# Optimization experiments

Hardware: AMD Instinct MI355X
Metric: run time of the kernel (lower is better)

The kernel has to match this reference:

```python
import jax, jax.numpy as jnp
import numpy as np

N_NODES = 100000
N_EDGES = 1000000
N_GRAPHS = 128
IN_DIM, HID, LAT, N_LAYERS = 32, 64, 32, 3


def setup_inputs() -> dict:
    key = jax.random.key(0)
    ks = jax.random.split(key, 10)
    x = jax.random.normal(ks[0], (N_NODES, IN_DIM), dtype=jnp.float32)
    edge_index = jax.random.randint(ks[1], (2, N_EDGES), 0, N_NODES, dtype=jnp.int64)
    batch = jnp.sort(jax.random.randint(ks[2], (N_NODES,), 0, N_GRAPHS, dtype=jnp.int64))
    s_in = 1.0 / np.sqrt(IN_DIM)
    s_h = 1.0 / np.sqrt(HID)
    return {
        "x": x,
        "edge_index": edge_index,
        "batch": batch,
        "w_in": jax.random.normal(ks[3], (IN_DIM, HID), dtype=jnp.float32) * s_in,
        "b_in": jnp.zeros((HID,), jnp.float32),
        "w1": jax.random.normal(ks[4], (N_LAYERS, HID, HID), dtype=jnp.float32) * s_h,
        "b1": jnp.zeros((N_LAYERS, HID), jnp.float32),
        "w2": jax.random.normal(ks[5], (N_LAYERS, HID, HID), dtype=jnp.float32) * s_h,
        "b2": jnp.zeros((N_LAYERS, HID), jnp.float32),
        "w_fc": jax.random.normal(ks[6], (HID, LAT), dtype=jnp.float32) * s_h,
        "b_fc": jnp.zeros((LAT,), jnp.float32),
    }


def reference(x, edge_index, batch, w_in, b_in, w1, b1, w2, b2, w_fc, b_fc):
    # Input projection: [N, in] -> [N, H]
    h = x @ w_in + b_in
    src, dst = edge_index[0], edge_index[1]
    for i in range(N_LAYERS):
        h_skip = h
        # GINConv (eps=0): aggregate neighbor sum then MLP
        agg = jax.ops.segment_sum(h[src], dst, num_segments=N_NODES)  # [N, H]
        m = h + agg
        m = jax.nn.relu(m @ w1[i] + b1[i])
        m = jax.nn.relu(m @ w2[i] + b2[i])
        # dropout is identity in eval mode; residual skip
        h = m + h_skip
    # global_add_pool over graphs
    pooled = jax.ops.segment_sum(h, batch, num_segments=N_GRAPHS)  # [G, H]
    return pooled @ w_fc + b_fc
```

## Files before the change

### kernel.cpp

```cpp
#include <hip/hip_runtime.h>

#define N_NODES 100000
#define N_EDGES 1000000
#define N_GRAPHS 128
#define IN_DIM 32
#define HID 64
#define LAT 32
#define N_LAYERS 3

#define MPAD 68
#define NB_SUM ((N_NODES + 255) / 256)

__global__ __launch_bounds__(256) void proj_kernel(
    const float* __restrict__ x, const float* __restrict__ w_in,
    const float* __restrict__ b_in, float* __restrict__ h) {
    __shared__ float ws[IN_DIM * HID];
    __shared__ float xs[4 * IN_DIM];
    int tid = threadIdx.x;
    for (int i = tid; i < IN_DIM * HID / 4; i += 256)
        ((float4*)ws)[i] = ((const float4*)w_in)[i];
    if (tid < 32) {
        int r = tid >> 3, c4 = tid & 7;
        int nn = blockIdx.x * 4 + r;
        float4 v = make_float4(0.f, 0.f, 0.f, 0.f);
        if (nn < N_NODES) v = ((const float4*)(x + (size_t)nn * IN_DIM))[c4];
        ((float4*)xs)[tid] = v;
    }
    __syncthreads();
    int w = tid >> 6, j = tid & 63;
    int n = blockIdx.x * 4 + w;
    if (n >= N_NODES) return;
    float acc = b_in[j];
#pragma unroll
    for (int k = 0; k < IN_DIM; k += 4) {
        float4 xv = *(const float4*)&xs[w * IN_DIM + k];
        acc += xv.x * ws[(k + 0) * HID + j];
        acc += xv.y * ws[(k + 1) * HID + j];
        acc += xv.z * ws[(k + 2) * HID + j];
        acc += xv.w * ws[(k + 3) * HID + j];
    }
    h[(size_t)n * HID + j] = acc;
}

__global__ __launch_bounds__(256) void hist_kernel(const int* __restrict__ ei,
                                                   int* __restrict__ counts) {
    int e = blockIdx.x * 256 + threadIdx.x;
    if (e < N_EDGES) atomicAdd(&counts[ei[N_EDGES + e]], 1);
}

__global__ __launch_bounds__(256) void block_sum_kernel(
    const int* __restrict__ counts, int* __restrict__ bsums) {
    __shared__ int sd[4];
    int i = blockIdx.x * 256 + threadIdx.x;
    int v = (i < N_NODES) ? counts[i] : 0;
#pragma unroll
    for (int off = 32; off >= 1; off >>= 1) v += __shfl_down(v, off);
    int lane = threadIdx.x & 63, w = threadIdx.x >> 6;
    if (lane == 0) sd[w] = v;
    __syncthreads();
    if (threadIdx.x == 0) bsums[blockIdx.x] = sd[0] + sd[1] + sd[2] + sd[3];
}

__global__ __launch_bounds__(256) void scan_bsums_kernel(
    const int* __restrict__ bsums, int* __restrict__ bofs, int nb) {
    __shared__ int tmp[256];
    __shared__ int carry;
    int tid = threadIdx.x;
    if (tid == 0) carry = 0;
    __syncthreads();
    for (int base = 0; base < nb; base += 256) {
        int v = (base + tid < nb) ? bsums[base + tid] : 0;
        tmp[tid] = v;
        __syncthreads();
        for (int off = 1; off < 256; off <<= 1) {
            int t = (tid >= off) ? tmp[tid - off] : 0;
            __syncthreads();
            tmp[tid] += t;
            __syncthreads();
        }
        if (base + tid < nb) bofs[base + tid] = carry + tmp[tid] - v;
        __syncthreads();
        if (tid == 255) carry += tmp[255];
        __syncthreads();
    }
}

__global__ __launch_bounds__(256) void offsets_kernel(
    const int* __restrict__ counts, const int* __restrict__ bofs,
    int* __restrict__ offsets, int* __restrict__ cursor) {
    __shared__ int tmp[256];
    int tid = threadIdx.x;
    int i = blockIdx.x * 256 + tid;
    int v = (i < N_NODES) ? counts[i] : 0;
    tmp[tid] = v;
    __syncthreads();
    for (int off = 1; off < 256; off <<= 1) {
        int t = (tid >= off) ? tmp[tid - off] : 0;
        __syncthreads();
        tmp[tid] += t;
        __syncthreads();
    }
    int excl = tmp[tid] - v + bofs[blockIdx.x];
    if (i < N_NODES) {
        offsets[i] = excl;
        cursor[i] = excl;
        if (i == N_NODES - 1) offsets[N_NODES] = excl + v;
    }
}

__global__ __launch_bounds__(256) void fill_kernel(const int* __restrict__ ei,
                                                   int* __restrict__ cursor,
                                                   int* __restrict__ srcs) {
    int e = blockIdx.x * 256 + threadIdx.x;
    if (e < N_EDGES) {
        int d = ei[N_EDGES + e];
        int p = atomicAdd(&cursor[d], 1);
        srcs[p] = ei[e];
    }
}

__global__ __launch_bounds__(256) void gather_kernel(
    const int* __restrict__ offsets, const int* __restrict__ srcs,
    const float* __restrict__ h, float* __restrict__ agg) {
    int w = threadIdx.x >> 6, j = threadIdx.x & 63;
    int n = blockIdx.x * 4 + w;
    if (n >= N_NODES) return;
    int beg = offsets[n], end = offsets[n + 1];
    float acc0 = 0.f, acc1 = 0.f, acc2 = 0.f, acc3 = 0.f;
    for (int c = beg; c < end; c += 64) {
        int myS = (c + j < end) ? srcs[c + j] : 0;
        int m = min(64, end - c);
        int i = 0;
        for (; i + 3 < m; i += 4) {
            int s0 = __shfl(myS, i);
            int s1 = __shfl(myS, i + 1);
            int s2 = __shfl(myS, i + 2);
            int s3 = __shfl(myS, i + 3);
            acc0 += h[(size_t)s0 * HID + j];
            acc1 += h[(size_t)s1 * HID + j];
            acc2 += h[(size_t)s2 * HID + j];
            acc3 += h[(size_t)s3 * HID + j];
        }
        for (; i < m; i++) acc0 += h[(size_t)__shfl(myS, i) * HID + j];
    }
    agg[(size_t)n * HID + j] = acc0 + acc1 + acc2 + acc3;
}

__global__ __launch_bounds__(512) void mlp_kernel(
    float* __restrict__ h, const float* __restrict__ agg,
    const float* __restrict__ w1, const float* __restrict__ b1,
    const float* __restrict__ w2, const float* __restrict__ b2) {
    __shared__ float w1s[HID * HID];
    __shared__ float w2s[HID * HID];
    __shared__ float ms[64 * MPAD];
    int tid = threadIdx.x;
    int row0 = blockIdx.x * 64;
    for (int i = tid; i < HID * HID / 4; i += 512) {
        ((float4*)w1s)[i] = ((const float4*)w1)[i];
        ((float4*)w2s)[i] = ((const float4*)w2)[i];
    }
#pragma unroll
    for (int i = 0; i < 2; i++) {
        int f = tid + i * 512;
        int r = f >> 4, c4 = f & 15;
        int n = row0 + r;
        float4 mv = make_float4(0.f, 0.f, 0.f, 0.f);
        if (n < N_NODES) {
            float4 h4 = ((const float4*)(h + (size_t)n * HID))[c4];
            float4 a4 = ((const float4*)(agg + (size_t)n * HID))[c4];
            mv = make_float4(h4.x + a4.x, h4.y + a4.y, h4.z + a4.z, h4.w + a4.w);
        }
        *(float4*)&ms[r * MPAD + c4 * 4] = mv;
    }
    __syncthreads();

    int ty = tid >> 4, tx = tid & 15;
    int r0 = ty * 2, c0 = tx * 4;

    float4 a0, a1;
#define GEMM_LDS(WS)                                                          \
    do {                                                                      \
        a0 = make_float4(0.f, 0.f, 0.f, 0.f); a1 = a0;                        \
        _Pragma("unroll 4")                                                   \
        for (int k0 = 0; k0 < HID; k0 += 4) {                                 \
            float4 m0 = *(const float4*)&ms[(r0 + 0) * MPAD + k0];            \
            float4 m1 = *(const float4*)&ms[(r0 + 1) * MPAD + k0];            \
            float4 w0 = *(const float4*)&WS[(k0 + 0) * HID + c0];             \
            float4 w1v = *(const float4*)&WS[(k0 + 1) * HID + c0];            \
            float4 w2v = *(const float4*)&WS[(k0 + 2) * HID + c0];            \
            float4 w3v = *(const float4*)&WS[(k0 + 3) * HID + c0];            \
            a0.x += m0.x * w0.x + m0.y * w1v.x + m0.z * w2v.x + m0.w * w3v.x; \
            a0.y += m0.x * w0.y + m0.y * w1v.y + m0.z * w2v.y + m0.w * w3v.y; \
            a0.z += m0.x * w0.z + m0.y * w1v.z + m0.z * w2v.z + m0.w * w3v.z; \
            a0.w += m0.x * w0.w + m0.y * w1v.w + m0.z * w2v.w + m0.w * w3v.w; \
            a1.x += m1.x * w0.x + m1.y * w1v.x + m1.z * w2v.x + m1.w * w3v.x; \
            a1.y += m1.x * w0.y + m1.y * w1v.y + m1.z * w2v.y + m1.w * w3v.y; \
            a1.z += m1.x * w0.z + m1.y * w1v.z + m1.z * w2v.z + m1.w * w3v.z; \
            a1.w += m1.x * w0.w + m1.y * w1v.w + m1.z * w2v.w + m1.w * w3v.w; \
        }                                                                     \
    } while (0)

    GEMM_LDS(w1s);

    float4 bv1 = *(const float4*)&b1[c0];
    float4 t0 = make_float4(fmaxf(a0.x + bv1.x, 0.f), fmaxf(a0.y + bv1.y, 0.f),
                            fmaxf(a0.z + bv1.z, 0.f), fmaxf(a0.w + bv1.w, 0.f));
    float4 t1 = make_float4(fmaxf(a1.x + bv1.x, 0.f), fmaxf(a1.y + bv1.y, 0.f),
                            fmaxf(a1.z + bv1.z, 0.f), fmaxf(a1.w + bv1.w, 0.f));

    __syncthreads();
    *(float4*)&ms[(r0 + 0) * MPAD + c0] = t0;
    *(float4*)&ms[(r0 + 1) * MPAD + c0] = t1;
    __syncthreads();

    GEMM_LDS(w2s);

    float4 bv2 = *(const float4*)&b2[c0];
#pragma unroll
    for (int i = 0; i < 2; i++) {
        int n = row0 + r0 + i;
        if (n < N_NODES) {
            float4 av = (i == 0) ? a0 : a1;
            float4 hold = *(const float4*)(h + (size_t)n * HID + c0);
            float4 o;
            o.x = fmaxf(av.x + bv2.x, 0.f) + hold.x;
            o.y = fmaxf(av.y + bv2.y, 0.f) + hold.y;
            o.z = fmaxf(av.z + bv2.z, 0.f) + hold.z;
            o.w = fmaxf(av.w + bv2.w, 0.f) + hold.w;
            *(float4*)(h + (size_t)n * HID + c0) = o;
        }
    }
#undef GEMM_LDS
}

__global__ __launch_bounds__(256) void pool_kernel(
    const float* __restrict__ h, const int* __restrict__ batch,
    float* __restrict__ pooled) {
    int tid = threadIdx.x;
    int w = tid >> 6, j = tid & 63;
    int n0 = blockIdx.x * 256 + w * 64;
    if (n0 >= N_NODES) return;
    int nend = min(n0 + 64, N_NODES);
    float acc = 0.f;
    int cur = batch[n0];
    for (int n = n0; n < nend; n++) {
        int b = batch[n];
        if (b != cur) {
            atomicAdd(&pooled[cur * HID + j], acc);
            acc = 0.f;
            cur = b;
        }
        acc += h[(size_t)n * HID + j];
    }
    atomicAdd(&pooled[cur * HID + j], acc);
}

__global__ __launch_bounds__(256) void final_kernel(
    const float* __restrict__ pooled, const float* __restrict__ w_fc,
    const float* __restrict__ b_fc, float* __restrict__ out) {
    int gid = blockIdx.x * 256 + threadIdx.x;
    if (gid >= N_GRAPHS * LAT) return;
    int g = gid >> 5, j = gid & 31;
    float acc = b_fc[j];
#pragma unroll
    for (int k = 0; k < HID; k++)
        acc += pooled[g * HID + k] * w_fc[k * LAT + j];
    out[gid] = acc;
}

extern "C" void kernel_launch(void* const* d_in, const int* in_sizes, int n_in,
                              void* d_out, int out_size, void* d_ws,
                              size_t ws_size, hipStream_t stream) {
    const float* x     = (const float*)d_in[0];
    const int*   ei    = (const int*)d_in[1];
    const int*   batch = (const int*)d_in[2];
    const float* w_in  = (const float*)d_in[3];
    const float* b_in  = (const float*)d_in[4];
    const float* w1    = (const float*)d_in[5];
    const float* b1    = (const float*)d_in[6];
    const float* w2    = (const float*)d_in[7];
    const float* b2    = (const float*)d_in[8];
    const float* w_fc  = (const float*)d_in[9];
    const float* b_fc  = (const float*)d_in[10];
    float* out = (float*)d_out;

    float* h       = (float*)d_ws;
    float* agg     = h + (size_t)N_NODES * HID;
    float* pooled  = agg + (size_t)N_NODES * HID;
    int*   offsets = (int*)(pooled + N_GRAPHS * HID);
    int*   srcs    = offsets + (N_NODES + 2);
    int* counts = (int*)agg;
    int* cursor = counts + N_NODES;
    int* bsums  = cursor + N_NODES;
    int* bofs   = bsums + (NB_SUM + 1);

    proj_kernel<<<(N_NODES + 3) / 4, 256, 0, stream>>>(x, w_in, b_in, h);

    hipMemsetAsync(counts, 0, N_NODES * sizeof(int), stream);
    hist_kernel<<<(N_EDGES + 255) / 256, 256, 0, stream>>>(ei, counts);
    block_sum_kernel<<<NB_SUM, 256, 0, stream>>>(counts, bsums);
    scan_bsums_kernel<<<1, 256, 0, stream>>>(bsums, bofs, NB_SUM);
    offsets_kernel<<<NB_SUM, 256, 0, stream>>>(counts, bofs, offsets, cursor);
    fill_kernel<<<(N_EDGES + 255) / 256, 256, 0, stream>>>(ei, cursor, srcs);

    for (int i = 0; i < N_LAYERS; i++) {
        gather_kernel<<<(N_NODES + 3) / 4, 256, 0, stream>>>(offsets, srcs, h, agg);
        mlp_kernel<<<(N_NODES + 63) / 64, 512, 0, stream>>>(
            h, agg, w1 + (size_t)i * HID * HID, b1 + (size_t)i * HID,
            w2 + (size_t)i * HID * HID, b2 + (size_t)i * HID);
    }

    hipMemsetAsync(pooled, 0, N_GRAPHS * HID * sizeof(float), stream);
    pool_kernel<<<(N_NODES + 255) / 256, 256, 0, stream>>>(h, batch, pooled);
    final_kernel<<<(N_GRAPHS * LAT + 255) / 256, 256, 0, stream>>>(
        pooled, w_fc, b_fc, out);
}
```

Baseline: 480.9 us.

## Replace per-node CSR build with bucketed bin sort and LDS-atomic aggregation

Instead of building a full CSR (histogram, multi-kernel scan, atomic fill), edges are sorted into coarse buckets of 256 destination nodes using per-block LDS staging, packing the local destination and source into one int. Aggregation then runs one block per bucket, summing neighbor features into a shared-memory tile with LDS float atomics and writing the tile out coalesced. This aims to cut global atomic scatter and several launches from preprocessing. In exchange it uses 64 KB of LDS per block, launches few blocks, and adds LDS atomic contention and nondeterministic summation order.

```diff
diff --git a/kernel.cpp b/kernel.cpp
--- a/kernel.cpp
+++ b/kernel.cpp
@@ -9,7 +9,11 @@
 #define N_LAYERS 3
 
 #define MPAD 68
-#define NB_SUM ((N_NODES + 255) / 256)
+
+#define BSZ 256
+#define NBK ((N_NODES + BSZ - 1) / BSZ)
+#define EPB 16384
+#define NBIN_BLOCKS ((N_EDGES + EPB - 1) / EPB)
 
 __global__ __launch_bounds__(256) void proj_kernel(
     const float* __restrict__ x, const float* __restrict__ w_in,
@@ -42,108 +46,138 @@
     h[(size_t)n * HID + j] = acc;
 }
 
-__global__ __launch_bounds__(256) void hist_kernel(const int* __restrict__ ei,
-                                                   int* __restrict__ counts) {
-    int e = blockIdx.x * 256 + threadIdx.x;
-    if (e < N_EDGES) atomicAdd(&counts[ei[N_EDGES + e]], 1);
-}
-
-__global__ __launch_bounds__(256) void block_sum_kernel(
-    const int* __restrict__ counts, int* __restrict__ bsums) {
-    __shared__ int sd[4];
-    int i = blockIdx.x * 256 + threadIdx.x;
-    int v = (i < N_NODES) ? counts[i] : 0;
-#pragma unroll
-    for (int off = 32; off >= 1; off >>= 1) v += __shfl_down(v, off);
-    int lane = threadIdx.x & 63, w = threadIdx.x >> 6;
-    if (lane == 0) sd[w] = v;
-    __syncthreads();
-    if (threadIdx.x == 0) bsums[blockIdx.x] = sd[0] + sd[1] + sd[2] + sd[3];
-}
-
-__global__ __launch_bounds__(256) void scan_bsums_kernel(
-    const int* __restrict__ bsums, int* __restrict__ bofs, int nb) {
-    __shared__ int tmp[256];
-    __shared__ int carry;
-    int tid = threadIdx.x;
-    if (tid == 0) carry = 0;
-    __syncthreads();
-    for (int base = 0; base < nb; base += 256) {
-        int v = (base + tid < nb) ? bsums[base + tid] : 0;
-        tmp[tid] = v;
+__global__ __launch_bounds__(256) void bhist_kernel(const int* __restrict__ ei,
+                                                    int* __restrict__ bhist) {
+    __shared__ int hs[NBK];
+    for (int i = threadIdx.x; i < NBK; i += 256) hs[i] = 0;
+    __syncthreads();
+    int e = blockIdx.x * (256 * 16) + threadIdx.x;
+#pragma unroll
+    for (int k = 0; k < 16; k++, e += 256)
+        if (e < N_EDGES) atomicAdd(&hs[ei[N_EDGES + e] >> 8], 1);
+    __syncthreads();
+    for (int i = threadIdx.x; i < NBK; i += 256) {
+        int c = hs[i];
+        if (c) atomicAdd(&bhist[i], c);
+    }
+}
+
+__global__ __launch_bounds__(512) void bscan_kernel(const int* __restrict__ bhist,
+                                                    int* __restrict__ bstart,
+                                                    int* __restrict__ bcursor) {
+    __shared__ int sc[512];
+    int tid = threadIdx.x;
+    int v = (tid < NBK) ? bhist[tid] : 0;
+    sc[tid] = v;
+    __syncthreads();
+    for (int off = 1; off < 512; off <<= 1) {
+        int t = (tid >= off) ? sc[tid - off] : 0;
         __syncthreads();
-        for (int off = 1; off < 256; off <<= 1) {
-            int t = (tid >= off) ? tmp[tid - off] : 0;
-            __syncthreads();
-            tmp[tid] += t;
-            __syncthreads();
-        }
-        if (base + tid < nb) bofs[base + tid] = carry + tmp[tid] - v;
+        sc[tid] += t;
         __syncthreads();
-        if (tid == 255) carry += tmp[255];
+    }
+    if (tid < NBK) {
+        int ex = sc[tid] - v;
+        bstart[tid] = ex;
+        bcursor[tid] = ex;
+    }
+    if (tid == 0) bstart[NBK] = N_EDGES;
+}
+
+__global__ __launch_bounds__(512) void binsort_kernel(const int* __restrict__ ei,
+                                                      int* __restrict__ bcursor,
+                                                      int* __restrict__ tmp) {
+    __shared__ int hist[NBK];
+    __shared__ int lofs[NBK + 1];
+    __shared__ int cur[NBK];
+    __shared__ int gbase[NBK];
+    __shared__ int sc[512];
+    __shared__ int stage[EPB];
+    int tid = threadIdx.x;
+    int e0 = blockIdx.x * EPB;
+    int nE = min(EPB, N_EDGES - e0);
+    for (int i = tid; i < NBK; i += 512) hist[i] = 0;
+    __syncthreads();
+    for (int i = tid; i < nE; i += 512)
+        atomicAdd(&hist[ei[N_EDGES + e0 + i] >> 8], 1);
+    __syncthreads();
+    int v = (tid < NBK) ? hist[tid] : 0;
+    sc[tid] = v;
+    __syncthreads();
+    for (int off = 1; off < 512; off <<= 1) {
+        int t = (tid >= off) ? sc[tid - off] : 0;
         __syncthreads();
-    }
-}
-
-__global__ __launch_bounds__(256) void offsets_kernel(
-    const int* __restrict__ counts, const int* __restrict__ bofs,
-    int* __restrict__ offsets, int* __restrict__ cursor) {
-    __shared__ int tmp[256];
-    int tid = threadIdx.x;
-    int i = blockIdx.x * 256 + tid;
-    int v = (i < N_NODES) ? counts[i] : 0;
-    tmp[tid] = v;
-    __syncthreads();
-    for (int off = 1; off < 256; off <<= 1) {
-        int t = (tid >= off) ? tmp[tid - off] : 0;
+        sc[tid] += t;
         __syncthreads();
-        tmp[tid] += t;
-        __syncthreads();
-    }
-    int excl = tmp[tid] - v + bofs[blockIdx.x];
-    if (i < N_NODES) {
-        offsets[i] = excl;
-        cursor[i] = excl;
-        if (i == N_NODES - 1) offsets[N_NODES] = excl + v;
-    }
-}
-
-__global__ __launch_bounds__(256) void fill_kernel(const int* __restrict__ ei,
-                                                   int* __restrict__ cursor,
-                                                   int* __restrict__ srcs) {
-    int e = blockIdx.x * 256 + threadIdx.x;
-    if (e < N_EDGES) {
-        int d = ei[N_EDGES + e];
-        int p = atomicAdd(&cursor[d], 1);
-        srcs[p] = ei[e];
-    }
-}
-
-__global__ __launch_bounds__(256) void gather_kernel(
-    const int* __restrict__ offsets, const int* __restrict__ srcs,
+    }
+    if (tid < NBK) {
+        int ex = sc[tid] - v;
+        lofs[tid] = ex;
+        cur[tid] = ex;
+        gbase[tid] = atomicAdd(&bcursor[tid], v);
+    }
+    if (tid == 0) lofs[NBK] = nE;
+    __syncthreads();
+    for (int i = tid; i < nE; i += 512) {
+        int s = ei[e0 + i];
+        int d = ei[N_EDGES + e0 + i];
+        int b = d >> 8;
+        int p = atomicAdd(&cur[b], 1);
+        stage[p] = ((d & 255) << 17) | s;
+    }
+    __syncthreads();
+    for (int i = tid; i < nE; i += 512) {
+        int pv = stage[i];
+        int lo = 0, hi = NBK;
+        while (hi - lo > 1) {
+            int mid = (lo + hi) >> 1;
+            if (lofs[mid] <= i) lo = mid; else hi = mid;
+        }
+        tmp[gbase[lo] + (i - lofs[lo])] = pv;
+    }
+}
+
+__global__ __launch_bounds__(512) void gather_agg_kernel(
+    const int* __restrict__ bstart, const int* __restrict__ tmp,
     const float* __restrict__ h, float* __restrict__ agg) {
-    int w = threadIdx.x >> 6, j = threadIdx.x & 63;
-    int n = blockIdx.x * 4 + w;
-    if (n >= N_NODES) return;
-    int beg = offsets[n], end = offsets[n + 1];
-    float acc0 = 0.f, acc1 = 0.f, acc2 = 0.f, acc3 = 0.f;
-    for (int c = beg; c < end; c += 64) {
-        int myS = (c + j < end) ? srcs[c + j] : 0;
-        int m = min(64, end - c);
+    __shared__ float aggS[BSZ * HID];
+    int tid = threadIdx.x;
+    int b = blockIdx.x;
+    for (int i = tid; i < BSZ * HID / 4; i += 512)
+        ((float4*)aggS)[i] = make_float4(0.f, 0.f, 0.f, 0.f);
+    int beg = bstart[b], end = bstart[b + 1];
+    __syncthreads();
+    int w = tid >> 6, j = tid & 63;
+    for (int c = beg + w * 64; c < end; c += 64 * 8) {
+        int nE = min(64, end - c);
+        int myP = (j < nE) ? tmp[c + j] : 0;
         int i = 0;
-        for (; i + 3 < m; i += 4) {
-            int s0 = __shfl(myS, i);
-            int s1 = __shfl(myS, i + 1);
-            int s2 = __shfl(myS, i + 2);
-            int s3 = __shfl(myS, i + 3);
-            acc0 += h[(size_t)s0 * HID + j];
-            acc1 += h[(size_t)s1 * HID + j];
-            acc2 += h[(size_t)s2 * HID + j];
-            acc3 += h[(size_t)s3 * HID + j];
-        }
-        for (; i < m; i++) acc0 += h[(size_t)__shfl(myS, i) * HID + j];
-    }
-    agg[(size_t)n * HID + j] = acc0 + acc1 + acc2 + acc3;
+        for (; i + 3 < nE; i += 4) {
+            int p0 = __shfl(myP, i);
+            int p1 = __shfl(myP, i + 1);
+            int p2 = __shfl(myP, i + 2);
+            int p3 = __shfl(myP, i + 3);
+            float v0 = h[(size_t)(p0 & 0x1FFFF) * HID + j];
+            float v1 = h[(size_t)(p1 & 0x1FFFF) * HID + j];
+            float v2 = h[(size_t)(p2 & 0x1FFFF) * HID + j];
+            float v3 = h[(size_t)(p3 & 0x1FFFF) * HID + j];
+            atomicAdd(&aggS[(p0 >> 17) * HID + j], v0);
+            atomicAdd(&aggS[(p1 >> 17) * HID + j], v1);
+            atomicAdd(&aggS[(p2 >> 17) * HID + j], v2);
+            atomicAdd(&aggS[(p3 >> 17) * HID + j], v3);
+        }
+        for (; i < nE; i++) {
+            int p = __shfl(myP, i);
+            atomicAdd(&aggS[(p >> 17) * HID + j],
+                      h[(size_t)(p & 0x1FFFF) * HID + j]);
+        }
+    }
+    __syncthreads();
+    int n0 = b * BSZ;
+    int nn = min(BSZ, N_NODES - n0);
+    float4* dst4 = (float4*)(agg + (size_t)n0 * HID);
+    for (int i = tid; i < nn * (HID / 4); i += 512)
+        dst4[i] = ((const float4*)aggS)[i];
 }
 
 __global__ __launch_bounds__(512) void mlp_kernel(
@@ -287,24 +321,20 @@
     float* h       = (float*)d_ws;
     float* agg     = h + (size_t)N_NODES * HID;
     float* pooled  = agg + (size_t)N_NODES * HID;
-    int*   offsets = (int*)(pooled + N_GRAPHS * HID);
-    int*   srcs    = offsets + (N_NODES + 2);
-    int* counts = (int*)agg;
-    int* cursor = counts + N_NODES;
-    int* bsums  = cursor + N_NODES;
-    int* bofs   = bsums + (NB_SUM + 1);
+    int*   tmp     = (int*)(pooled + N_GRAPHS * HID);
+    int*   bhist   = tmp + N_EDGES;
+    int*   bstart  = bhist + NBK;
+    int*   bcursor = bstart + (NBK + 1);
 
     proj_kernel<<<(N_NODES + 3) / 4, 256, 0, stream>>>(x, w_in, b_in, h);
 
-    hipMemsetAsync(counts, 0, N_NODES * sizeof(int), stream);
-    hist_kernel<<<(N_EDGES + 255) / 256, 256, 0, stream>>>(ei, counts);
-    block_sum_kernel<<<NB_SUM, 256, 0, stream>>>(counts, bsums);
-    scan_bsums_kernel<<<1, 256, 0, stream>>>(bsums, bofs, NB_SUM);
-    offsets_kernel<<<NB_SUM, 256, 0, stream>>>(counts, bofs, offsets, cursor);
-    fill_kernel<<<(N_EDGES + 255) / 256, 256, 0, stream>>>(ei, cursor, srcs);
+    hipMemsetAsync(bhist, 0, NBK * sizeof(int), stream);
+    bhist_kernel<<<(N_EDGES + 4095) / 4096, 256, 0, stream>>>(ei, bhist);
+    bscan_kernel<<<1, 512, 0, stream>>>(bhist, bstart, bcursor);
+    binsort_kernel<<<NBIN_BLOCKS, 512, 0, stream>>>(ei, bcursor, tmp);
 
     for (int i = 0; i < N_LAYERS; i++) {
-        gather_kernel<<<(N_NODES + 3) / 4, 256, 0, stream>>>(offsets, srcs, h, agg);
+        gather_agg_kernel<<<NBK, 512, 0, stream>>>(bstart, tmp, h, agg);
         mlp_kernel<<<(N_NODES + 63) / 64, 512, 0, stream>>>(
             h, agg, w1 + (size_t)i * HID * HID, b1 + (size_t)i * HID,
             w2 + (size_t)i * HID * HID, b2 + (size_t)i * HID);
```

New measurement: 1.617 ms. 3.36x slower.
